# Kernel tuning notes

Hardware: AMD Instinct MI355X
Metric: run time of the kernel (lower is better)

The kernel has to match this reference:

```python
import jax, jax.numpy as jnp
import numpy as np

N = 256          # spatial_dim
NC = 3           # components: u, v, density
INNER = 10       # inner_steps
DX = 2.0 * np.pi / N
VISC = 1e-3


def _van_leer(r):
    # classic van Leer limiter: (r+|r|)/(1+|r|)
    return jnp.where(r > 0, 2.0 * r / (1.0 + r), 0.0)


def _advect(c, u, v, dt):
    """van-Leer flux-limited advection tendency -div(vel*c) on a periodic grid.
    TVD blend of upwind (low-order) and Lax-Wendroff (high-order) face fluxes."""
    tend = jnp.zeros_like(c)
    for ax, vel in ((-2, u), (-1, v)):
        uf = 0.5 * (vel + jnp.roll(vel, -1, ax))   # face velocity at i+1/2
        cn = jnp.roll(c, -1, ax)
        dc = cn - c
        f_low = jnp.where(uf >= 0, uf * c, uf * cn)                      # upwind
        f_high = uf * 0.5 * (c + cn) - 0.5 * uf * uf * (dt / DX) * dc    # Lax-Wendroff
        dc_up = jnp.where(uf >= 0, c - jnp.roll(c, 1, ax), jnp.roll(c, -2, ax) - cn)
        dc_safe = jnp.where(jnp.abs(dc) > 1e-12, dc, 1e-12)
        phi = _van_leer(dc_up / dc_safe)
        flux = f_low + phi * (f_high - f_low)
        tend = tend - (flux - jnp.roll(flux, 1, ax)) / DX
    return tend


def _laplacian(x):
    return (jnp.roll(x, 1, -1) + jnp.roll(x, -1, -1)
            + jnp.roll(x, 1, -2) + jnp.roll(x, -1, -2) - 4.0 * x) / (DX * DX)


def _inv_fd_laplacian_eigs():
    # eigenvalues of the periodic FD laplacian, pseudo-inverse (zero mean mode)
    k = np.arange(N)
    lam1 = (2.0 * np.cos(2.0 * np.pi * k / N) - 2.0) / (DX * DX)
    lam = lam1[:, None] + lam1[None, :]
    lam[0, 0] = 1.0
    inv = 1.0 / lam
    inv[0, 0] = 0.0
    return jnp.asarray(inv, dtype=jnp.float32)

_INV_LAM = _inv_fd_laplacian_eigs()


def _project(u, v):
    """Pressure projection: remove divergence via FFT Poisson solve (periodic)."""
    div = (u - jnp.roll(u, 1, -2)) / DX + (v - jnp.roll(v, 1, -1)) / DX  # backward diff
    q = jnp.real(jnp.fft.ifft2(jnp.fft.fft2(div) * _INV_LAM))
    gu = (jnp.roll(q, -1, -2) - q) / DX   # forward diff (adjoint of div)
    gv = (jnp.roll(q, -1, -1) - q) / DX
    return u - gu, v - gv


def _inner_step(state, dt):
    u, v, d = state
    # velocity: explicit van-Leer convection + explicit diffusion, then projection
    u1 = u + dt * (_advect(u, u, v, dt) + VISC * _laplacian(u))
    v1 = v + dt * (_advect(v, u, v, dt) + VISC * _laplacian(v))
    u1, v1 = _project(u1, v1)
    # density advected with the OLD velocity (matches module's inner_step_fn)
    d1 = d + dt * _advect(d, u, v, dt)
    return (u1, v1, d1)


def _repeated_step(state, dt):
    def body(s, _):
        return _inner_step(s, dt), None
    state, _ = jax.lax.scan(body, state, None, length=INNER)
    return state


def setup_inputs() -> dict:
    key = jax.random.key(0)
    y0 = 0.1 * jax.random.normal(key, (8, N * N * NC), dtype=jnp.float32)
    return {"y0": y0, "dt": jnp.float32(1e-3), "num_steps_forward": 8}


def reference(y0, dt, num_steps_forward):
    spatial = y0.reshape(-1, N, N, NC)           # [B,H,W,3]
    state0 = (spatial[..., 0], spatial[..., 1], spatial[..., 2])

    def body(s, _):
        s2 = _repeated_step(s, dt)
        return s2, s2
    _, traj = jax.lax.scan(body, state0, None, length=num_steps_forward)
    yt = jnp.stack(traj, axis=-1)                # [T,B,H,W,3]
    yt = jnp.swapaxes(yt, 0, 1)                  # [B,T,H,W,3]
    return yt.reshape(yt.shape[0], yt.shape[1], N * N * NC)
```

## Files before the change

kernel.cpp:

```cpp
#include <hip/hip_runtime.h>
#include <hip/hip_bf16.h>


#define NN 256
#define NM 255
#define FIELD (NN*NN)
#define BATCH 8
#define TOTAL (BATCH*FIELD)
#define ROWF2 264

constexpr float RDX  = 40.743665431525205f;
constexpr float VISC = 1e-3f;

__device__ __forceinline__ int rev8(int x) { return (int)(__brev((unsigned)x) >> 24); }
__device__ __forceinline__ int pdx(int x)  { return x + (x >> 5); }

__device__ __forceinline__ void wave_sync() {
  asm volatile("" ::: "memory");
  __builtin_amdgcn_wave_barrier();
}

__device__ __forceinline__ float decode_dt(const unsigned* dtw) {
  unsigned w = dtw[0];
  float cf = __uint_as_float(w);
  float cb = __uint_as_float((w & 0xFFFFu) << 16);
  bool v32 = (cf > 1e-8f) && (cf < 1.0f);
  bool vbf = (cb > 1e-8f) && (cb < 1.0f);
  return v32 ? cf : (vbf ? cb : 1e-3f);
}

__device__ __forceinline__ float face_flux(float uf, float cm, float c0,
                                           float cp, float cpp, float hdtdx) {
  float dc = cp - c0;
  float f_low  = (uf >= 0.0f) ? uf*c0 : uf*cp;
  float f_high = uf*0.5f*(c0+cp) - hdtdx*uf*uf*dc;
  float dc_up  = (uf >= 0.0f) ? (c0 - cm) : (cpp - cp);
  float dc_safe = (fabsf(dc) > 1e-12f) ? dc : 1e-12f;
  float phi = (dc_up * dc_safe > 0.0f) ? (2.0f*dc_up/(dc_up + dc_safe)) : 0.0f;
  return f_low + phi*(f_high - f_low);
}

template<int NEED_VD>
__device__ __forceinline__ void advect_point(
    const float* __restrict__ Ub, const float* __restrict__ Vb,
    const float* __restrict__ Db,
    int i, int j, float hdtdx, float dt,
    float& u1, float& v1, float& d1)
{
  int im2 = ((i-2)&NM)*NN, im1 = ((i-1)&NM)*NN, i0r = i*NN,
      ip1 = ((i+1)&NM)*NN, ip2 = ((i+2)&NM)*NN;
  int jm2 = (j-2)&NM, jm1 = (j-1)&NM, jp1 = (j+1)&NM, jp2 = (j+2)&NM;

  float u_c  = Ub[i0r+j];
  float u_im2= Ub[im2+j], u_im1 = Ub[im1+j], u_ip1 = Ub[ip1+j], u_ip2 = Ub[ip2+j];
  float u_jm2= Ub[i0r+jm2], u_jm1 = Ub[i0r+jm1], u_jp1 = Ub[i0r+jp1], u_jp2 = Ub[i0r+jp2];
  float v_c  = Vb[i0r+j];
  float v_jm1= Vb[i0r+jm1], v_jp1 = Vb[i0r+jp1];

  float ufI0 = 0.5f*(u_c + u_ip1);
  float ufIm = 0.5f*(u_im1 + u_c);
  float vfJ0 = 0.5f*(v_c + v_jp1);
  float vfJm = 0.5f*(v_jm1 + v_c);

  float tu = -(( face_flux(ufI0, u_im1, u_c, u_ip1, u_ip2, hdtdx)
               - face_flux(ufIm, u_im2, u_im1, u_c, u_ip1, hdtdx))
             + ( face_flux(vfJ0, u_jm1, u_c, u_jp1, u_jp2, hdtdx)
               - face_flux(vfJm, u_jm2, u_jm1, u_c, u_jp1, hdtdx))) * RDX;
  float lapu = (u_im1 + u_ip1 + u_jm1 + u_jp1 - 4.0f*u_c) * (RDX*RDX);
  u1 = u_c + dt*(tu + VISC*lapu);

  if (NEED_VD) {
    float v_im2= Vb[im2+j], v_im1 = Vb[im1+j], v_ip1 = Vb[ip1+j], v_ip2 = Vb[ip2+j];
    float v_jm2= Vb[i0r+jm2], v_jp2 = Vb[i0r+jp2];
    float d_c  = Db[i0r+j];
    float d_im2= Db[im2+j], d_im1 = Db[im1+j], d_ip1 = Db[ip1+j], d_ip2 = Db[ip2+j];
    float d_jm2= Db[i0r+jm2], d_jm1 = Db[i0r+jm1], d_jp1 = Db[i0r+jp1], d_jp2 = Db[i0r+jp2];

    float tv = -(( face_flux(ufI0, v_im1, v_c, v_ip1, v_ip2, hdtdx)
                 - face_flux(ufIm, v_im2, v_im1, v_c, v_ip1, hdtdx))
               + ( face_flux(vfJ0, v_jm1, v_c, v_jp1, v_jp2, hdtdx)
                 - face_flux(vfJm, v_jm2, v_jm1, v_c, v_jp1, hdtdx))) * RDX;
    float lapv = (v_im1 + v_ip1 + v_jm1 + v_jp1 - 4.0f*v_c) * (RDX*RDX);
    v1 = v_c + dt*(tv + VISC*lapv);

    float td = -(( face_flux(ufI0, d_im1, d_c, d_ip1, d_ip2, hdtdx)
                 - face_flux(ufIm, d_im2, d_im1, d_c, d_ip1, hdtdx))
               + ( face_flux(vfJ0, d_jm1, d_c, d_jp1, d_jp2, hdtdx)
                 - face_flux(vfJm, d_jm2, d_jm1, d_c, d_jp1, hdtdx))) * RDX;
    d1 = d_c + dt*td;
  }
}

template<int NEED_VD>
__device__ __forceinline__ void advect_point_lds(
    const float* __restrict__ U, const float* __restrict__ V,
    const float* __restrict__ D,
    int ku, int kv, int j, float hdtdx, float dt,
    float& u1, float& v1, float& d1)
{
  int jm2 = (j-2)&NM, jm1 = (j-1)&NM, jp1 = (j+1)&NM, jp2 = (j+2)&NM;

  const float* Ur = U + ku*NN;
  float u_c  = Ur[j];
  float u_im2= U[(ku-2)*NN+j], u_im1 = U[(ku-1)*NN+j],
        u_ip1= U[(ku+1)*NN+j], u_ip2 = U[(ku+2)*NN+j];
  float u_jm2= Ur[jm2], u_jm1 = Ur[jm1], u_jp1 = Ur[jp1], u_jp2 = Ur[jp2];
  const float* Vr = V + kv*NN;
  float v_c  = Vr[j];
  float v_jm1= Vr[jm1], v_jp1 = Vr[jp1];

  float ufI0 = 0.5f*(u_c + u_ip1);
  float ufIm = 0.5f*(u_im1 + u_c);
  float vfJ0 = 0.5f*(v_c + v_jp1);
  float vfJm = 0.5f*(v_jm1 + v_c);

  float tu = -(( face_flux(ufI0, u_im1, u_c, u_ip1, u_ip2, hdtdx)
               - face_flux(ufIm, u_im2, u_im1, u_c, u_ip1, hdtdx))
             + ( face_flux(vfJ0, u_jm1, u_c, u_jp1, u_jp2, hdtdx)
               - face_flux(vfJm, u_jm2, u_jm1, u_c, u_jp1, hdtdx))) * RDX;
  float lapu = (u_im1 + u_ip1 + u_jm1 + u_jp1 - 4.0f*u_c) * (RDX*RDX);
  u1 = u_c + dt*(tu + VISC*lapu);

  if (NEED_VD) {
    float v_im2= V[(kv-2)*NN+j], v_im1 = V[(kv-1)*NN+j],
          v_ip1= V[(kv+1)*NN+j], v_ip2 = V[(kv+2)*NN+j];
    float v_jm2= Vr[jm2], v_jp2 = Vr[jp2];
    const float* Dr = D + kv*NN;
    float d_c  = Dr[j];
    float d_im2= D[(kv-2)*NN+j], d_im1 = D[(kv-1)*NN+j],
          d_ip1= D[(kv+1)*NN+j], d_ip2 = D[(kv+2)*NN+j];
    float d_jm2= Dr[jm2], d_jm1 = Dr[jm1], d_jp1 = Dr[jp1], d_jp2 = Dr[jp2];

    float tv = -(( face_flux(ufI0, v_im1, v_c, v_ip1, v_ip2, hdtdx)
                 - face_flux(ufIm, v_im2, v_im1, v_c, v_ip1, hdtdx))
               + ( face_flux(vfJ0, v_jm1, v_c, v_jp1, v_jp2, hdtdx)
                 - face_flux(vfJm, v_jm2, v_jm1, v_c, v_jp1, hdtdx))) * RDX;
    float lapv = (v_im1 + v_ip1 + v_jm1 + v_jp1 - 4.0f*v_c) * (RDX*RDX);
    v1 = v_c + dt*(tv + VISC*lapv);

    float td = -(( face_flux(ufI0, d_im1, d_c, d_ip1, d_ip2, hdtdx)
                 - face_flux(ufIm, d_im2, d_im1, d_c, d_ip1, hdtdx))
               + ( face_flux(vfJ0, d_jm1, d_c, d_jp1, d_jp2, hdtdx)
                 - face_flux(vfJm, d_jm2, d_jm1, d_c, d_jp1, hdtdx))) * RDX;
    d1 = d_c + dt*td;
  }
}


__device__ __forceinline__ void fft256_fwd_f2(float2* __restrict__ A, int lane,
                                              const float2* __restrict__ tw,
                                              bool active)
{
  #pragma unroll
  for (int s = 1; s <= 8; s += 2) {
    if (active) {
      int half = 1 << (s-1);
      int q2 = lane & (half - 1);
      int i0 = ((lane >> (s-1)) << (s+1)) + q2;
      float2 a0 = A[pdx(i0)];
      float2 a1 = A[pdx(i0 + half)];
      float2 a2 = A[pdx(i0 + 2*half)];
      float2 a3 = A[pdx(i0 + 3*half)];
      float2 w1 = tw[q2 << (8 - s)];
      float wbx = w1.x*a1.x - w1.y*a1.y, wby = w1.x*a1.y + w1.y*a1.x;
      float2 b0 = make_float2(a0.x + wbx, a0.y + wby);
      float2 b1 = make_float2(a0.x - wbx, a0.y - wby);
      wbx = w1.x*a3.x - w1.y*a3.y; wby = w1.x*a3.y + w1.y*a3.x;
      float2 b2 = make_float2(a2.x + wbx, a2.y + wby);
      float2 b3 = make_float2(a2.x - wbx, a2.y - wby);
      float2 w2 = tw[q2 << (7 - s)];
      float2 w3 = tw[(q2 + half) << (7 - s)];
      wbx = w2.x*b2.x - w2.y*b2.y; wby = w2.x*b2.y + w2.y*b2.x;
      A[pdx(i0)]            = make_float2(b0.x + wbx, b0.y + wby);
      A[pdx(i0 + 2*half)]   = make_float2(b0.x - wbx, b0.y - wby);
      wbx = w3.x*b3.x - w3.y*b3.y; wby = w3.x*b3.y + w3.y*b3.x;
      A[pdx(i0 + half)]     = make_float2(b1.x + wbx, b1.y + wby);
      A[pdx(i0 + 3*half)]   = make_float2(b1.x - wbx, b1.y - wby);
    }
    wave_sync();
  }
}

__device__ __forceinline__ void fft256_inv_f2(float2* __restrict__ A, int lane,
                                              const float2* __restrict__ tw,
                                              bool active)
{
  #pragma unroll
  for (int s = 8; s >= 2; s -= 2) {
    if (active) {
      int h = 1 << (s-2);
      int q2 = lane & (h - 1);
      int i0 = ((lane >> (s-2)) << s) + q2;
      float2 a0 = A[pdx(i0)];
      float2 a1 = A[pdx(i0 + h)];
      float2 a2 = A[pdx(i0 + 2*h)];
      float2 a3 = A[pdx(i0 + 3*h)];
      float2 w1 = tw[q2 << (8 - s)];
      float2 w2 = tw[(q2 + h) << (8 - s)];
      float dx = a0.x - a2.x, dy = a0.y - a2.y;
      float2 b0 = make_float2(a0.x + a2.x, a0.y + a2.y);
      float2 b2 = make_float2(w1.x*dx + w1.y*dy, w1.x*dy - w1.y*dx);
      dx = a1.x - a3.x; dy = a1.y - a3.y;
      float2 b1 = make_float2(a1.x + a3.x, a1.y + a3.y);
      float2 b3 = make_float2(w2.x*dx + w2.y*dy, w2.x*dy - w2.y*dx);
      float2 w3 = tw[q2 << (9 - s)];
      dx = b0.x - b1.x; dy = b0.y - b1.y;
      A[pdx(i0)]       = make_float2(b0.x + b1.x, b0.y + b1.y);
      A[pdx(i0 + h)]   = make_float2(w3.x*dx + w3.y*dy, w3.x*dy - w3.y*dx);
      dx = b2.x - b3.x; dy = b2.y - b3.y;
      A[pdx(i0 + 2*h)] = make_float2(b2.x + b3.x, b2.y + b3.y);
      A[pdx(i0 + 3*h)] = make_float2(w3.x*dx + w3.y*dy, w3.x*dy - w3.y*dx);
    }
    wave_sync();
  }
}

template<int W>
__device__ __forceinline__ void fft256_dit_fwd(float2* __restrict__ A, int lane,
                                               const float2* __restrict__ tw,
                                               bool active)
{
  #pragma unroll
  for (int s = 1; s <= 8; ++s) {
    int half = 1 << (s-1);
    if (active) {
      #pragma unroll
      for (int r = 0; r < 128/W; ++r) {
        int bfly = lane + r*W;
        int q = bfly & (half - 1);
        int g = (bfly >> (s-1)) << s;
        float2 w = tw[q << (8 - s)];
        float2 a = A[pdx(g + q)];
        float2 b = A[pdx(g + q + half)];
        float wbx = w.x*b.x - w.y*b.y;
        float wby = w.x*b.y + w.y*b.x;
        A[pdx(g + q)]        = make_float2(a.x + wbx, a.y + wby);
        A[pdx(g + q + half)] = make_float2(a.x - wbx, a.y - wby);
      }
    }
    wave_sync();
  }
}

template<int W>
__device__ __forceinline__ void fft256_dif_inv(float2* __restrict__ A, int lane,
                                               const float2* __restrict__ tw,
                                               bool active)
{
  #pragma unroll
  for (int s = 8; s >= 1; --s) {
    int half = 1 << (s-1);
    if (active) {
      #pragma unroll
      for (int r = 0; r < 128/W; ++r) {
        int bfly = lane + r*W;
        int q = bfly & (half - 1);
        int g = (bfly >> (s-1)) << s;
        float2 w = tw[q << (8 - s)];
        float2 a = A[pdx(g + q)];
        float2 b = A[pdx(g + q + half)];
        float dx = a.x - b.x, dy = a.y - b.y;
        A[pdx(g + q)]        = make_float2(a.x + b.x, a.y + b.y);
        A[pdx(g + q + half)] = make_float2(w.x*dx + w.y*dy, w.x*dy - w.y*dx);
      }
    }
    wave_sync();
  }
}

__global__ __launch_bounds__(1024) void proj_advect_fft8(
    const float2* __restrict__ Sprev, const float* __restrict__ inb,
    float* __restrict__ outb, float2* __restrict__ Snew,
    float* __restrict__ out, const unsigned* __restrict__ dtw,
    int T, int tm1, int first)
{
  __shared__ float2 tw[128];
  __shared__ float2 AbS[14*ROWF2];
  __shared__ float  qs [14*NN];
  __shared__ float  Ucs[13*NN];
  __shared__ float  Vcs[12*NN];
  float* Dss = (float*)(AbS + 8*ROWF2);
  float* Vs  = qs;

  const int tid  = threadIdx.x;
  const int j    = tid & 255;
  const int qtr  = tid >> 8;
  const int b    = blockIdx.x >> 5;
  const int row0 = (blockIdx.x & 31) << 3;

  if (tid < 128) {
    float sw, cw;
    __sincosf(-0.02454369260617026f * (float)tid, &sw, &cw);
    tw[tid] = make_float2(cw, sw);
  }

  const float dt = decode_dt(dtw);
  const float hdtdx = 0.5f*dt*RDX;

  const float* Ub = inb + b*FIELD;
  const float* Vb = inb + TOTAL + b*FIELD;
  const float* Db = inb + 2*TOTAL + b*FIELD;
  float* Uo  = outb + b*FIELD;
  float* Vo  = outb + TOTAL + b*FIELD;
  float* Do_ = outb + 2*TOTAL + b*FIELD;

  float u_reg[4], v_reg[3], d_reg[3];
  #pragma unroll
  for (int m = 0; m < 4; ++m) {
    int e = tid + (m << 10);
    if (e < 13*NN) {
      int k = e >> 8, jj = e & 255;
      u_reg[m] = Ub[((row0 - 3 + k) & NM)*NN + jj];
    }
  }
  #pragma unroll
  for (int m = 0; m < 3; ++m) {
    int e = tid + (m << 10);
    int k = e >> 8, jj = e & 255;
    int gr = ((row0 - 2 + k) & NM)*NN;
    v_reg[m] = Vb[gr + jj];
    d_reg[m] = Db[gr + jj];
  }

  if (!first) {
    const float2* Sb = Sprev + b*FIELD;
    #pragma unroll
    for (int m = 0; m < 4; ++m) {
      int e = tid + (m << 10);
      if (e < 14*NN) {
        int k = e >> 8, jj = e & 255;
        AbS[k*ROWF2 + pdx(jj)] = Sb[((row0 - 3 + k) & NM)*NN + jj];
      }
    }
    __syncthreads();

    int g = tid >> 6, lane = tid & 63;
    bool act = (g < 14);
    fft256_inv_f2(AbS + (act ? g : 13)*ROWF2, lane, tw, act);
    __syncthreads();

    #pragma unroll
    for (int m = 0; m < 4; ++m) {
      int e = tid + (m << 10);
      if (e < 14*NN) {
        int k = e >> 8, jj = e & 255;
        qs[k*NN + jj] = AbS[k*ROWF2 + pdx(rev8(jj))].x;
      }
    }
    __syncthreads();
  } else {
    __syncthreads();
  }

  #pragma unroll
  for (int m = 0; m < 4; ++m) {
    int e = tid + (m << 10);
    if (e < 13*NN) {
      int k = e >> 8, jj = e & 255;
      Ucs[e] = first ? u_reg[m]
                     : (u_reg[m] - (qs[(k+1)*NN + jj] - qs[k*NN + jj])*RDX);
    }
  }
  #pragma unroll
  for (int m = 0; m < 3; ++m) {
    int e = tid + (m << 10);
    int k = e >> 8, jj = e & 255;
    Vcs[e] = first ? v_reg[m]
                   : (v_reg[m] - (qs[(k+1)*NN + ((jj+1)&NM)] - qs[(k+1)*NN + jj])*RDX);
    Dss[e] = d_reg[m];
  }
  __syncthreads();

  if (tm1 >= 0) {
    #pragma unroll
    for (int m = 0; m < 2; ++m) {
      int e = tid + (m << 10);
      int k = e >> 8, jj = e & 255;
      int pos = (row0 + k)*NN + jj;
      size_t o = ((size_t)(b*T + tm1)*FIELD + pos)*3u;
      out[o]   = Ucs[(k+3)*NN + jj];
      out[o+1] = Vcs[(k+2)*NN + jj];
      out[o+2] = Dss[(k+2)*NN + jj];
    }
  }

  const int kbeg = (qtr << 1) - 1;
  float u1r[3];
  #pragma unroll
  for (int kk = 0; kk < 3; ++kk) {
    int k = kbeg + kk;
    int ku = k + 3, kv = k + 2;
    float u1, v1, d1;
    if (kk == 0) {
      advect_point_lds<0>(Ucs, Vcs, Dss, ku, kv, j, hdtdx, dt, u1, v1, d1);
    } else {
      advect_point_lds<1>(Ucs, Vcs, Dss, ku, kv, j, hdtdx, dt, u1, v1, d1);
      int gi = (row0 + k)*NN + j;
      Uo[gi] = u1; Vo[gi] = v1; Do_[gi] = d1;
      Vs[k*NN + j] = v1;
    }
    u1r[kk] = u1;
  }
  __syncthreads();

  {
    int jm1 = (j - 1) & NM, rj = rev8(j);
    #pragma unroll
    for (int m = 0; m < 2; ++m) {
      int k = (qtr << 1) + m;
      float dv = (u1r[m+1] - u1r[m] + Vs[k*NN + j] - Vs[k*NN + jm1]) * RDX;
      AbS[k*ROWF2 + pdx(rj)] = make_float2(dv, 0.0f);
    }
  }
  __syncthreads();

  {
    const int g = tid >> 6, lane = tid & 63;
    bool act = (g < 8);
    fft256_fwd_f2(AbS + (act ? g : 7)*ROWF2, lane, tw, act);
  }
  __syncthreads();

  float2* So = Snew + b*FIELD;
  #pragma unroll
  for (int m = 0; m < 2; ++m) {
    int e = tid + (m << 10);
    int row = e >> 8, jj = e & 255;
    So[(row0 + row)*NN + jj] = AbS[row*ROWF2 + pdx(jj)];
  }
}

__global__ __launch_bounds__(512) void fft_cols(float2* __restrict__ S)
{
  __shared__ float2 Ab[8*ROWF2];
  __shared__ float2 tw[128];
  __shared__ float  lam[NN];
  int tid = threadIdx.x;
  int b = blockIdx.x >> 5;
  int col0 = (blockIdx.x & 31) << 3;

  if (tid < 128) {
    float sw, cw;
    __sincosf(-0.02454369260617026f * (float)tid, &sw, &cw);
    tw[tid] = make_float2(cw, sw);
  }
  if (tid < 256) {
    float s1 = __sinf(0.01227184630308512983f * (float)tid);
    lam[tid] = -4.0f * s1 * s1 * (RDX*RDX);
  }

  float2* Sb = S + b*FIELD;
  #pragma unroll
  for (int k = 0; k < 4; ++k) {
    int idx = tid + (k << 9);
    int i = idx >> 3, c = idx & 7;
    Ab[c*ROWF2 + pdx(rev8(i))] = Sb[i*NN + col0 + c];
  }
  __syncthreads();

  int g = tid >> 6, lane = tid & 63;
  fft256_fwd_f2(Ab + g*ROWF2, lane, tw, true);

  float l2 = lam[col0 + g];
  #pragma unroll
  for (int r = 0; r < 4; ++r) {
    int k1 = lane + (r << 6);
    float den = lam[k1] + l2;
    float sc = ((k1 | (col0 + g)) == 0) ? 0.0f : (1.0f/den);
    sc *= (1.0f/65536.0f);
    float2 v = Ab[g*ROWF2 + pdx(k1)];
    Ab[g*ROWF2 + pdx(k1)] = make_float2(v.x*sc, v.y*sc);
  }
  wave_sync();

  fft256_inv_f2(Ab + g*ROWF2, lane, tw, true);
  __syncthreads();

  #pragma unroll
  for (int k = 0; k < 4; ++k) {
    int idx = tid + (k << 9);
    int i = idx >> 3, c = idx & 7;
    Sb[i*NN + col0 + c] = Ab[c*ROWF2 + pdx(rev8(i))];
  }
}

__global__ __launch_bounds__(512) void advect_div_fft(
    const float* __restrict__ inb, float* __restrict__ outb,
    float2* __restrict__ S, float* __restrict__ out,
    const unsigned* __restrict__ dtw, int T, int tm1)
{
  __shared__ float  Vs[8][NN];
  __shared__ float2 AbS[8*ROWF2];
  __shared__ float2 tw[128];
  const int tid = threadIdx.x;
  const int j   = tid & 255;
  const int h   = tid >> 8;
  const int b    = blockIdx.x >> 5;
  const int row0 = (blockIdx.x & 31) << 3;

  if (tid < 128) {
    float sw, cw;
    __sincosf(-0.02454369260617026f * (float)tid, &sw, &cw);
    tw[tid] = make_float2(cw, sw);
  }

  const float* Ub = inb + b*FIELD;
  const float* Vb = inb + TOTAL + b*FIELD;
  const float* Db = inb + 2*TOTAL + b*FIELD;
  float* Uo  = outb + b*FIELD;
  float* Vo  = outb + TOTAL + b*FIELD;
  float* Do_ = outb + 2*TOTAL + b*FIELD;

  const float dt = decode_dt(dtw);
  const float hdtdx = 0.5f*dt*RDX;

  if (tm1 >= 0) {
    #pragma unroll
    for (int k = 0; k < 4; ++k) {
      int pos = (row0 + h*4 + k)*NN + j;
      size_t o = ((size_t)(b*T + tm1)*FIELD + pos)*3u;
      out[o]   = Ub[pos];
      out[o+1] = Vb[pos];
      out[o+2] = Db[pos];
    }
  }

  const int kbeg = h ? 3 : -1;
  float u1r[5];
  #pragma unroll
  for (int kk = 0; kk < 5; ++kk) {
    int k = kbeg + kk;
    int r = (row0 + k) & NM;
    float u1, v1, d1;
    if (kk == 0) {
      advect_point<0>(Ub, Vb, Db, r, j, hdtdx, dt, u1, v1, d1);
    } else {
      advect_point<1>(Ub, Vb, Db, r, j, hdtdx, dt, u1, v1, d1);
      int gi = r*NN + j;
      Uo[gi] = u1; Vo[gi] = v1; Do_[gi] = d1;
      Vs[k][j] = v1;
    }
    u1r[kk] = u1;
  }
  __syncthreads();

  {
    int jm1 = (j - 1) & NM, rj = rev8(j);
    #pragma unroll
    for (int m = 0; m < 4; ++m) {
      int k = h*4 + m;
      float dv = (u1r[m+1] - u1r[m] + Vs[k][j] - Vs[k][jm1]) * RDX;
      AbS[k*ROWF2 + pdx(rj)] = make_float2(dv, 0.0f);
    }
  }
  __syncthreads();

  const int g = tid >> 6, lane = tid & 63;
  fft256_dit_fwd<64>(AbS + g*ROWF2, lane, tw, true);
  __syncthreads();

  float2* Sb = S + b*FIELD;
  #pragma unroll
  for (int k = 0; k < 4; ++k) {
    int row = h*4 + k;
    Sb[(row0 + row)*NN + j] = AbS[row*ROWF2 + pdx(j)];
  }
}

__global__ __launch_bounds__(512) void fft_cols_r9(float2* __restrict__ S)
{
  __shared__ float2 Ab[8*ROWF2];
  __shared__ float2 tw[128];
  __shared__ float  lam[NN];
  int tid = threadIdx.x;
  int b = blockIdx.x >> 5;
  int col0 = (blockIdx.x & 31) << 3;

  if (tid < 128) {
    float sw, cw;
    __sincosf(-0.02454369260617026f * (float)tid, &sw, &cw);
    tw[tid] = make_float2(cw, sw);
  }
  if (tid < 256) {
    float s1 = __sinf(0.01227184630308512983f * (float)tid);
    lam[tid] = -4.0f * s1 * s1 * (RDX*RDX);
  }

  float2* Sb = S + b*FIELD;
  #pragma unroll
  for (int k = 0; k < 4; ++k) {
    int idx = tid + (k << 9);
    int i = idx >> 3, c = idx & 7;
    Ab[c*ROWF2 + pdx(rev8(i))] = Sb[i*NN + col0 + c];
  }
  __syncthreads();

  int g = tid >> 6, lane = tid & 63;
  fft256_dit_fwd<64>(Ab + g*ROWF2, lane, tw, true);

  float l2 = lam[col0 + g];
  #pragma unroll
  for (int r = 0; r < 4; ++r) {
    int k1 = lane + (r << 6);
    float den = lam[k1] + l2;
    float sc = ((k1 | (col0 + g)) == 0) ? 0.0f : (1.0f/den);
    sc *= (1.0f/65536.0f);
    float2 v = Ab[g*ROWF2 + pdx(k1)];
    Ab[g*ROWF2 + pdx(k1)] = make_float2(v.x*sc, v.y*sc);
  }
  wave_sync();

  fft256_dif_inv<64>(Ab + g*ROWF2, lane, tw, true);
  __syncthreads();

  #pragma unroll
  for (int k = 0; k < 4; ++k) {
    int idx = tid + (k << 9);
    int i = idx >> 3, c = idx & 7;
    Sb[i*NN + col0 + c] = Ab[c*ROWF2 + pdx(rev8(i))];
  }
}

__global__ __launch_bounds__(512) void fft_inv_correct(
    const float2* __restrict__ S, float* __restrict__ outb)
{
  __shared__ float2 Ab[9*ROWF2];
  __shared__ float  qs[9*NN];
  __shared__ float2 tw[128];
  int tid = threadIdx.x;
  int b = blockIdx.x >> 5;
  int row0 = (blockIdx.x & 31) << 3;

  if (tid < 128) {
    float sw, cw;
    __sincosf(-0.02454369260617026f * (float)tid, &sw, &cw);
    tw[tid] = make_float2(cw, sw);
  }

  const float2* Sb = S + b*FIELD;
  #pragma unroll
  for (int m = 0; m < 5; ++m) {
    int e = tid + m*512;
    if (e < 9*NN) {
      int k = e >> 8, j = e & 255;
      Ab[k*ROWF2 + pdx(j)] = Sb[((row0 + k) & NM)*NN + j];
    }
  }
  __syncthreads();

  int g = tid >> 5, lane = tid & 31;
  bool active = (g < 9);
  fft256_dif_inv<32>(Ab + (active ? g : 8)*ROWF2, lane, tw, active);
  __syncthreads();

  #pragma unroll
  for (int m = 0; m < 5; ++m) {
    int e = tid + m*512;
    if (e < 9*NN) {
      int k = e >> 8, j = e & 255;
      qs[k*NN + j] = Ab[k*ROWF2 + pdx(rev8(j))].x;
    }
  }
  __syncthreads();

  float* Ug = outb + b*FIELD;
  float* Vg = outb + TOTAL + b*FIELD;
  #pragma unroll
  for (int m = 0; m < 4; ++m) {
    int e = tid + m*512;
    int k = e >> 8, j = e & 255;
    int gi = (row0 + k)*NN + j;
    float q0 = qs[k*NN + j];
    float q1 = qs[(k+1)*NN + j];
    float qj = qs[k*NN + ((j+1) & NM)];
    Ug[gi] -= (q1 - q0)*RDX;
    Vg[gi] -= (qj - q0)*RDX;
  }
}

__global__ __launch_bounds__(256) void write_out_k(
    const float* __restrict__ U, const float* __restrict__ V, const float* __restrict__ D,
    float* __restrict__ out, int t, int T)
{
  int idx = blockIdx.x*256 + threadIdx.x;
  int b = idx >> 16;
  int pos = idx & (FIELD-1);
  size_t o = ((size_t)(b*T + t)*FIELD + pos)*3u;
  out[o]   = U[idx];
  out[o+1] = V[idx];
  out[o+2] = D[idx];
}

__global__ __launch_bounds__(256) void init_state(
    const float* __restrict__ y0,
    float* __restrict__ U, float* __restrict__ V, float* __restrict__ D)
{
  int idx = blockIdx.x*256 + threadIdx.x;
  U[idx] = y0[idx*3];
  V[idx] = y0[idx*3+1];
  D[idx] = y0[idx*3+2];
}

__device__ __forceinline__ void fft_fwd_sc(float2* A, int lane) {
  #pragma unroll
  for (int s = 1; s <= 8; ++s) {
    int half = 1 << (s-1);
    float angscale = -6.28318530717958647692f / (float)(2*half);
    #pragma unroll
    for (int r = 0; r < 4; ++r) {
      int bfly = lane + (r << 5);
      int q = bfly & (half - 1);
      int g = (bfly >> (s-1)) << s;
      float sw, cw; __sincosf(angscale * (float)q, &sw, &cw);
      float2 a = A[g+q], b = A[g+q+half];
      float wbx = cw*b.x - sw*b.y, wby = cw*b.y + sw*b.x;
      A[g+q] = make_float2(a.x+wbx, a.y+wby);
      A[g+q+half] = make_float2(a.x-wbx, a.y-wby);
    }
    __syncthreads();
  }
}
__device__ __forceinline__ void fft_inv_sc(float2* A, int lane) {
  #pragma unroll
  for (int s = 8; s >= 1; --s) {
    int half = 1 << (s-1);
    float angscale = 6.28318530717958647692f / (float)(2*half);
    #pragma unroll
    for (int r = 0; r < 4; ++r) {
      int bfly = lane + (r << 5);
      int q = bfly & (half - 1);
      int g = (bfly >> (s-1)) << s;
      float sw, cw; __sincosf(angscale * (float)q, &sw, &cw);
      float2 a = A[g+q], b = A[g+q+half];
      float dx = a.x-b.x, dy = a.y-b.y;
      A[g+q] = make_float2(a.x+b.x, a.y+b.y);
      A[g+q+half] = make_float2(cw*dx - sw*dy, cw*dy + sw*dx);
    }
    __syncthreads();
  }
}

__global__ __launch_bounds__(256) void advect_kernel_fb(
    const float* __restrict__ U, const float* __restrict__ V, const float* __restrict__ D,
    float* __restrict__ Uo, float* __restrict__ Vo, float* __restrict__ Do_,
    const unsigned* __restrict__ dtw)
{
  int idx = blockIdx.x*256 + threadIdx.x;
  int j = idx & NM, i = (idx >> 8) & NM, base = (idx >> 16) * FIELD;
  float dt = decode_dt(dtw);
  float u1, v1, d1;
  advect_point<1>(U + base, V + base, D + base, i, j, 0.5f*dt*RDX, dt, u1, v1, d1);
  Uo[idx] = u1; Vo[idx] = v1; Do_[idx] = d1;
}

__global__ __launch_bounds__(256) void fft_rows_div_fb(
    const float* __restrict__ U2, const float* __restrict__ V2, float2* __restrict__ S)
{
  __shared__ float2 Ab[8*NN];
  int tid = threadIdx.x, b = blockIdx.x >> 5, row0 = (blockIdx.x & 31) << 3;
  const float* Ub = U2 + b*FIELD;
  const float* Vb = V2 + b*FIELD;
  int jm1 = (tid - 1) & NM, rj = rev8(tid);
  #pragma unroll
  for (int k = 0; k < 8; ++k) {
    int row = row0 + k, rm1 = (row - 1) & NM;
    float dv = (Ub[row*NN + tid] - Ub[rm1*NN + tid]
              + Vb[row*NN + tid] - Vb[row*NN + jm1]) * RDX;
    Ab[(k<<8) + rj] = make_float2(dv, 0.0f);
  }
  __syncthreads();
  int g = tid >> 5, lane = tid & 31;
  fft_fwd_sc(Ab + (g<<8), lane);
  float2* Sb = S + b*FIELD;
  #pragma unroll
  for (int k = 0; k < 8; ++k)
    Sb[(row0 + k)*NN + tid] = Ab[(k<<8) + tid];
}

__global__ __launch_bounds__(256) void fft_cols_fb(float2* __restrict__ S)
{
  __shared__ float2 Ab[8*NN];
  int tid = threadIdx.x, b = blockIdx.x >> 5, col0 = (blockIdx.x & 31) << 3;
  float2* Sb = S + b*FIELD;
  #pragma unroll
  for (int k = 0; k < 8; ++k) {
    int idx = tid + (k << 8);
    int i = idx >> 3, c = idx & 7;
    Ab[(c<<8) + rev8(i)] = Sb[i*NN + col0 + c];
  }
  __syncthreads();
  int g = tid >> 5, lane = tid & 31;
  fft_fwd_sc(Ab + (g<<8), lane);
  int k2 = col0 + g;
  float s2 = __sinf(0.01227184630308512983f * (float)k2);
  float l2 = -4.0f * s2 * s2 * (RDX*RDX);
  #pragma unroll
  for (int r = 0; r < 8; ++r) {
    int k1 = lane + (r << 5);
    float s1 = __sinf(0.01227184630308512983f * (float)k1);
    float l1 = -4.0f * s1 * s1 * (RDX*RDX);
    float den = l1 + l2;
    float sc = ((k1 | k2) == 0) ? 0.0f : (1.0f/den);
    sc *= (1.0f/65536.0f);
    float2 v = Ab[(g<<8) + k1];
    Ab[(g<<8) + k1] = make_float2(v.x*sc, v.y*sc);
  }
  __syncthreads();
  fft_inv_sc(Ab + (g<<8), lane);
  #pragma unroll
  for (int k = 0; k < 8; ++k) {
    int idx = tid + (k << 8);
    int i = idx >> 3, c = idx & 7;
    Sb[i*NN + col0 + c] = Ab[(c<<8) + rev8(i)];
  }
}

__global__ __launch_bounds__(256) void fft_rows_inv_fb(
    const float2* __restrict__ S, float* __restrict__ Q)
{
  __shared__ float2 Ab[8*NN];
  int tid = threadIdx.x, b = blockIdx.x >> 5, row0 = (blockIdx.x & 31) << 3;
  const float2* Sb = S + b*FIELD;
  #pragma unroll
  for (int k = 0; k < 8; ++k)
    Ab[(k<<8) + tid] = Sb[(row0 + k)*NN + tid];
  __syncthreads();
  int g = tid >> 5, lane = tid & 31;
  fft_inv_sc(Ab + (g<<8), lane);
  float* Qb = Q + b*FIELD;
  int rj = rev8(tid);
  #pragma unroll
  for (int k = 0; k < 8; ++k)
    Qb[(row0 + k)*NN + tid] = Ab[(k<<8) + rj].x;
}

__global__ __launch_bounds__(256) void correct_uv_fb(
    float* __restrict__ U2, float* __restrict__ V2, const float* __restrict__ Q)
{
  int idx = blockIdx.x*256 + threadIdx.x;
  int j = idx & NM, i = (idx >> 8) & NM, base = (idx >> 16) * FIELD;
  const float* Qb = Q + base;
  float q0 = Qb[i*NN + j];
  float qi = Qb[((i+1)&NM)*NN + j];
  float qj = Qb[i*NN + ((j+1)&NM)];
  U2[idx] -= (qi - q0)*RDX;
  V2[idx] -= (qj - q0)*RDX;
}

extern "C" void kernel_launch(void* const* d_in, const int* in_sizes, int n_in,
                              void* d_out, int out_size, void* d_ws, size_t ws_size,
                              hipStream_t stream) {
  (void)in_sizes; (void)n_in;
  const float*    y0  = (const float*)d_in[0];
  const unsigned* dtw = (const unsigned*)d_in[1];
  float* out = (float*)d_out;

  int T = out_size / (3*FIELD*BATCH);
  if (T < 1) T = 1;

  float* wsf = (float*)d_ws;

  if (ws_size >= (size_t)10*TOTAL*sizeof(float)) {
    float* stA = wsf;
    float* stB = wsf + 3*TOTAL;
    float2* Sa = (float2*)(wsf + 6*TOTAL);
    float2* Sc = (float2*)(wsf + 8*TOTAL);

    init_state<<<TOTAL/256, 256, 0, stream>>>(y0, stA, stA+TOTAL, stA+2*TOTAL);
    float* inb  = stA;
    float* outb = stB;
    float2* Sr = Sa;
    float2* Sw = Sc;
    int step = 0;
    for (int t = 0; t < T; ++t) {
      for (int s = 0; s < 10; ++s) {
        int tm1 = (s == 0) ? (t - 1) : -1;
        proj_advect_fft8<<<256, 1024, 0, stream>>>(Sr, inb, outb, Sw, out,
                                                   dtw, T, tm1, step == 0);
        fft_cols<<<256, 512, 0, stream>>>(Sw);
        float*  t1 = inb; inb = outb; outb = t1;
        float2* t2 = Sr;  Sr  = Sw;   Sw  = t2;
        ++step;
      }
    }
    fft_inv_correct<<<256, 512, 0, stream>>>(Sr, inb);
    write_out_k<<<TOTAL/256, 256, 0, stream>>>(inb, inb+TOTAL, inb+2*TOTAL,
                                               out, T-1, T);
    return;
  }

  if (ws_size >= (size_t)8*TOTAL*sizeof(float)) {
    float2* S = (float2*)(wsf + 6*TOTAL);
    init_state<<<TOTAL/256, 256, 0, stream>>>(y0, wsf, wsf+TOTAL, wsf+2*TOTAL);
    float* inb = wsf;
    float* outb = wsf + 3*TOTAL;
    for (int t = 0; t < T; ++t) {
      for (int s = 0; s < 10; ++s) {
        int tm1 = (s == 0) ? (t - 1) : -1;
        advect_div_fft <<<256, 512, 0, stream>>>(inb, outb, S, out, dtw, T, tm1);
        fft_cols_r9    <<<256, 512, 0, stream>>>(S);
        fft_inv_correct<<<256, 512, 0, stream>>>(S, outb);
        float* tmp = inb; inb = outb; outb = tmp;
      }
    }
    write_out_k<<<TOTAL/256, 256, 0, stream>>>(inb, inb+TOTAL, inb+2*TOTAL,
                                               out, T-1, T);
    return;
  }

  float* bank0 = wsf;
  float* bank1 = wsf + 3*TOTAL;
  init_state<<<TOTAL/256, 256, 0, stream>>>(y0, bank0, bank0+TOTAL, bank0+2*TOTAL);
  float* inb = bank0;
  float* outb = bank1;
  for (int t = 0; t < T; ++t) {
    for (int s = 0; s < 10; ++s) {
      float *Ui = inb,  *Vi = inb + TOTAL,  *Di = inb + 2*TOTAL;
      float *Uo = outb, *Vo = outb + TOTAL, *Do_ = outb + 2*TOTAL;
      float2* S = (float2*)(inb + TOTAL);
      float*  Q = inb;
      advect_kernel_fb<<<TOTAL/256, 256, 0, stream>>>(Ui, Vi, Di, Uo, Vo, Do_, dtw);
      fft_rows_div_fb <<<BATCH*32, 256, 0, stream>>>(Uo, Vo, S);
      fft_cols_fb     <<<BATCH*32, 256, 0, stream>>>(S);
      fft_rows_inv_fb <<<BATCH*32, 256, 0, stream>>>(S, Q);
      correct_uv_fb   <<<TOTAL/256, 256, 0, stream>>>(Uo, Vo, Q);
      float* tmp = inb; inb = outb; outb = tmp;
    }
    write_out_k<<<TOTAL/256, 256, 0, stream>>>(inb, inb+TOTAL, inb+2*TOTAL, out, t, T);
  }
}
```

Baseline: 2.043 ms.

## Replace per-wave radix-2 shared-memory FFT with register-blocked 16x16 decomposition

The column FFT, spectral Poisson scaling and inverse FFT move from a 64-lane-per-row radix-2 scheme, which passes through shared memory every two stages, to a 16-thread-per-row scheme. Each thread holds 16 points in registers and runs four butterfly stages locally, and shared memory is touched only at three exchange points. The scaling and the high-half inverse stages are fused in registers. Only 128 of the 512 threads are active in this phase, which cuts parallelism and adds register pressure in exchange for fewer LDS round-trips. The wave_sync between exchanges relies on each 16-thread group sitting inside a single wavefront.

```diff
diff --git a/kernel.cpp b/kernel.cpp
--- a/kernel.cpp
+++ b/kernel.cpp
@@ -146,6 +146,71 @@
   }
 }
 
+
+__device__ __forceinline__ void r16_fwd_low(float2* x, const float2* tw) {
+  #pragma unroll
+  for (int s = 1; s <= 4; ++s) {
+    int h = 1 << (s-1);
+    #pragma unroll
+    for (int b = 0; b < 8; ++b) {
+      int q = b & (h-1);
+      int t = ((b >> (s-1)) << s) + q;
+      float2 w = tw[q << (8-s)];
+      float2 a = x[t], c = x[t+h];
+      float wbx = w.x*c.x - w.y*c.y, wby = w.x*c.y + w.y*c.x;
+      x[t]   = make_float2(a.x+wbx, a.y+wby);
+      x[t+h] = make_float2(a.x-wbx, a.y-wby);
+    }
+  }
+}
+__device__ __forceinline__ void r16_fwd_high(float2* x, int r, const float2* tw) {
+  #pragma unroll
+  for (int s = 5; s <= 8; ++s) {
+    int hp = 1 << (s-5);
+    #pragma unroll
+    for (int b = 0; b < 8; ++b) {
+      int qp = b & (hp-1);
+      int t = ((b >> (s-5)) << (s-4)) + qp;
+      float2 w = tw[(r + (qp<<4)) << (8-s)];
+      float2 a = x[t], c = x[t+hp];
+      float wbx = w.x*c.x - w.y*c.y, wby = w.x*c.y + w.y*c.x;
+      x[t]    = make_float2(a.x+wbx, a.y+wby);
+      x[t+hp] = make_float2(a.x-wbx, a.y-wby);
+    }
+  }
+}
+__device__ __forceinline__ void r16_inv_high(float2* x, int r, const float2* tw) {
+  #pragma unroll
+  for (int s = 8; s >= 5; --s) {
+    int hp = 1 << (s-5);
+    #pragma unroll
+    for (int b = 0; b < 8; ++b) {
+      int qp = b & (hp-1);
+      int t = ((b >> (s-5)) << (s-4)) + qp;
+      float2 w = tw[(r + (qp<<4)) << (8-s)];
+      float2 a = x[t], c = x[t+hp];
+      float dx = a.x-c.x, dy = a.y-c.y;
+      x[t]    = make_float2(a.x+c.x, a.y+c.y);
+      x[t+hp] = make_float2(w.x*dx + w.y*dy, w.x*dy - w.y*dx);
+    }
+  }
+}
+__device__ __forceinline__ void r16_inv_low(float2* x, const float2* tw) {
+  #pragma unroll
+  for (int s = 4; s >= 1; --s) {
+    int h = 1 << (s-1);
+    #pragma unroll
+    for (int b = 0; b < 8; ++b) {
+      int q = b & (h-1);
+      int t = ((b >> (s-1)) << s) + q;
+      float2 w = tw[q << (8-s)];
+      float2 a = x[t], c = x[t+h];
+      float dx = a.x-c.x, dy = a.y-c.y;
+      x[t]   = make_float2(a.x+c.x, a.y+c.y);
+      x[t+h] = make_float2(w.x*dx + w.y*dy, w.x*dy - w.y*dx);
+    }
+  }
+}
 
 __device__ __forceinline__ void fft256_fwd_f2(float2* __restrict__ A, int lane,
                                               const float2* __restrict__ tw,
@@ -458,22 +523,51 @@
   }
   __syncthreads();
 
-  int g = tid >> 6, lane = tid & 63;
-  fft256_fwd_f2(Ab + g*ROWF2, lane, tw, true);
-
-  float l2 = lam[col0 + g];
-  #pragma unroll
-  for (int r = 0; r < 4; ++r) {
-    int k1 = lane + (r << 6);
-    float den = lam[k1] + l2;
-    float sc = ((k1 | (col0 + g)) == 0) ? 0.0f : (1.0f/den);
-    sc *= (1.0f/65536.0f);
-    float2 v = Ab[g*ROWF2 + pdx(k1)];
-    Ab[g*ROWF2 + pdx(k1)] = make_float2(v.x*sc, v.y*sc);
-  }
-  wave_sync();
-
-  fft256_inv_f2(Ab + g*ROWF2, lane, tw, true);
+  {
+    const int g = tid >> 4;
+    const int r = tid & 15;
+    const bool act = (tid < 128);
+    float2* Ar = Ab + g*ROWF2;
+
+    if (act) {
+      float2 x[16];
+      #pragma unroll
+      for (int t = 0; t < 16; ++t) x[t] = Ar[pdx((r<<4) + t)];
+      r16_fwd_low(x, tw);
+      #pragma unroll
+      for (int t = 0; t < 16; ++t) Ar[pdx((r<<4) + t)] = x[t];
+    }
+    wave_sync();
+
+    if (act) {
+      float2 x[16];
+      #pragma unroll
+      for (int k = 0; k < 16; ++k) x[k] = Ar[pdx(r + (k<<4))];
+      r16_fwd_high(x, r, tw);
+      float l2 = lam[col0 + g];
+      #pragma unroll
+      for (int k = 0; k < 16; ++k) {
+        int k1 = r + (k<<4);
+        float den = lam[k1] + l2;
+        float sc = ((k1 | (col0 + g)) == 0) ? 0.0f : (1.0f/den);
+        sc *= (1.0f/65536.0f);
+        x[k].x *= sc; x[k].y *= sc;
+      }
+      r16_inv_high(x, r, tw);
+      #pragma unroll
+      for (int k = 0; k < 16; ++k) Ar[pdx(r + (k<<4))] = x[k];
+    }
+    wave_sync();
+
+    if (act) {
+      float2 x[16];
+      #pragma unroll
+      for (int t = 0; t < 16; ++t) x[t] = Ar[pdx((r<<4) + t)];
+      r16_inv_low(x, tw);
+      #pragma unroll
+      for (int t = 0; t < 16; ++t) Ar[pdx((r<<4) + t)] = x[t];
+    }
+  }
   __syncthreads();
 
   #pragma unroll
```

New measurement: 2.078 ms. Within noise of the previous version (+1.7%).
